# Optimization experiments

Hardware: AMD Instinct MI355X
Metric: run time of the kernel (lower is better)

## Reference

```python
import jax, jax.numpy as jnp
import numpy as np
from jax import lax

DEPTH = 12
NUM_HEADS = 12
WINDOW = 14
GLOBAL_IDX = (2, 5, 8, 11)
EPS = 1e-6


def setup_inputs() -> dict:
    key = jax.random.key(0)
    ks = iter(jax.random.split(key, 64))
    def rn(shape, s=0.02):
        return jax.random.normal(next(ks), shape, jnp.float32) * s
    D, mlp, hd = 768, 3072, 64
    return dict(
        x=jax.random.normal(next(ks), (1, 3, 512, 512), jnp.float32),
        patch_w=rn((D, 3, 16, 16)), patch_b=rn((D,)),
        pos_embed=rn((1, 32, 32, D)),
        ln1_w=jnp.ones((DEPTH, D)), ln1_b=jnp.zeros((DEPTH, D)),
        qkv_w=rn((DEPTH, D, 3 * D)), qkv_b=rn((DEPTH, 3 * D)),
        proj_w=rn((DEPTH, D, D)), proj_b=rn((DEPTH, D)),
        ln2_w=jnp.ones((DEPTH, D)), ln2_b=jnp.zeros((DEPTH, D)),
        mlp1_w=rn((DEPTH, D, mlp)), mlp1_b=rn((DEPTH, mlp)),
        mlp2_w=rn((DEPTH, mlp, D)), mlp2_b=rn((DEPTH, D)),
        rel_h_win=rn((8, 2 * WINDOW - 1, hd)), rel_w_win=rn((8, 2 * WINDOW - 1, hd)),
        rel_h_glob=rn((4, 2 * 32 - 1, hd)), rel_w_glob=rn((4, 2 * 32 - 1, hd)),
        neck_w1=rn((256, D, 1, 1)),
        neck_ln1_w=jnp.ones((256,)), neck_ln1_b=jnp.zeros((256,)),
        neck_w2=rn((256, 256, 3, 3)),
        neck_ln2_w=jnp.ones((256,)), neck_ln2_b=jnp.zeros((256,)),
    )


def layer_norm(x, w, b):
    m = jnp.mean(x, -1, keepdims=True)
    v = jnp.mean(jnp.square(x - m), -1, keepdims=True)
    return (x - m) * lax.rsqrt(v + EPS) * w + b


def layer_norm_2d(x, w, b):
    # channels-first LN over dim 1, as in SAM's LayerNorm2d
    m = jnp.mean(x, 1, keepdims=True)
    v = jnp.mean(jnp.square(x - m), 1, keepdims=True)
    x = (x - m) * lax.rsqrt(v + EPS)
    return x * w[None, :, None, None] + b[None, :, None, None]


def window_partition(x, ws):
    B, H, W, C = x.shape
    ph, pw = (-H) % ws, (-W) % ws
    x = jnp.pad(x, ((0, 0), (0, ph), (0, pw), (0, 0)))
    Hp, Wp = H + ph, W + pw
    x = x.reshape(B, Hp // ws, ws, Wp // ws, ws, C).transpose(0, 1, 3, 2, 4, 5)
    return x.reshape(-1, ws, ws, C), (Hp, Wp)


def window_unpartition(win, ws, pad_hw, hw):
    Hp, Wp = pad_hw
    H, W = hw
    B = win.shape[0] // (Hp * Wp // ws // ws)
    x = win.reshape(B, Hp // ws, Wp // ws, ws, ws, -1).transpose(0, 1, 3, 2, 4, 5)
    x = x.reshape(B, Hp, Wp, -1)
    return x[:, :H, :W, :]


def attention(x, qkv_w, qkv_b, proj_w, proj_b, Rh, Rw):
    B, H, W, C = x.shape
    nh = NUM_HEADS
    hd = C // nh
    scale = hd ** -0.5
    qkv = (x.reshape(B, H * W, C) @ qkv_w + qkv_b).reshape(B, H * W, 3, nh, hd)
    qkv = qkv.transpose(2, 0, 3, 1, 4).reshape(3, B * nh, H * W, hd)
    q, k, v = qkv[0], qkv[1], qkv[2]
    attn = jnp.einsum('bqc,bkc->bqk', q * scale, k)  # (B*nh, HW, HW)
    # decomposed rel-pos (q_size == k_size, no interpolation branch)
    idx_h = jnp.arange(H)[:, None] - jnp.arange(H)[None, :] + (H - 1)
    idx_w = jnp.arange(W)[:, None] - jnp.arange(W)[None, :] + (W - 1)
    Rh_s = Rh[idx_h]  # (H, H, hd)
    Rw_s = Rw[idx_w]  # (W, W, hd)
    r_q = q.reshape(B * nh, H, W, hd)
    rel_h = jnp.einsum('bhwc,hkc->bhwk', r_q, Rh_s)
    rel_w = jnp.einsum('bhwc,wkc->bhwk', r_q, Rw_s)
    attn = attn.reshape(B * nh, H, W, H, W) + rel_h[:, :, :, :, None] + rel_w[:, :, :, None, :]
    attn = jax.nn.softmax(attn.reshape(B * nh, H * W, H * W), axis=-1)
    out = (attn @ v).reshape(B, nh, H, W, hd).transpose(0, 2, 3, 1, 4).reshape(B, H, W, C)
    return out @ proj_w + proj_b


def encoder_forward(x, patch_w, patch_b, pos_embed, ln1_w, ln1_b, qkv_w, qkv_b,
                    proj_w, proj_b, ln2_w, ln2_b, mlp1_w, mlp1_b, mlp2_w, mlp2_b,
                    rel_h_win, rel_w_win, rel_h_glob, rel_w_glob,
                    neck_w1, neck_ln1_w, neck_ln1_b, neck_w2, neck_ln2_w, neck_ln2_b):
    dn = ('NCHW', 'OIHW', 'NCHW')
    # patch embed: conv 16x16 stride 16 -> (B, H', W', C)
    h = lax.conv_general_dilated(x, patch_w, (16, 16), 'VALID', dimension_numbers=dn)
    h = h + patch_b[None, :, None, None]
    h = h.transpose(0, 2, 3, 1)  # (B, 32, 32, 768)
    h = h + pos_embed
    wi = gi = 0
    for i in range(DEPTH):
        shortcut = h
        y = layer_norm(h, ln1_w[i], ln1_b[i])
        if i in GLOBAL_IDX:
            y = attention(y, qkv_w[i], qkv_b[i], proj_w[i], proj_b[i],
                          rel_h_glob[gi], rel_w_glob[gi])
            gi += 1
        else:
            Hh, Ww = y.shape[1], y.shape[2]
            y, pad_hw = window_partition(y, WINDOW)
            y = attention(y, qkv_w[i], qkv_b[i], proj_w[i], proj_b[i],
                          rel_h_win[wi], rel_w_win[wi])
            y = window_unpartition(y, WINDOW, pad_hw, (Hh, Ww))
            wi += 1
        h = shortcut + y
        m = layer_norm(h, ln2_w[i], ln2_b[i])
        m = jax.nn.gelu(m @ mlp1_w[i] + mlp1_b[i], approximate=False) @ mlp2_w[i] + mlp2_b[i]
        h = h + m
    # neck
    h = h.transpose(0, 3, 1, 2)  # (B, C, H, W)
    h = lax.conv_general_dilated(h, neck_w1, (1, 1), 'VALID', dimension_numbers=dn)
    h = layer_norm_2d(h, neck_ln1_w, neck_ln1_b)
    h = lax.conv_general_dilated(h, neck_w2, (1, 1), [(1, 1), (1, 1)], dimension_numbers=dn)
    h = layer_norm_2d(h, neck_ln2_w, neck_ln2_b)
    return h  # (B, 256, 32, 32)


def reference(x, patch_w, patch_b, pos_embed, ln1_w, ln1_b, qkv_w, qkv_b,
              proj_w, proj_b, ln2_w, ln2_b, mlp1_w, mlp1_b, mlp2_w, mlp2_b,
              rel_h_win, rel_w_win, rel_h_glob, rel_w_glob,
              neck_w1, neck_ln1_w, neck_ln1_b, neck_w2, neck_ln2_w, neck_ln2_b):
    return encoder_forward(x, patch_w, patch_b, pos_embed, ln1_w, ln1_b, qkv_w, qkv_b,
                           proj_w, proj_b, ln2_w, ln2_b, mlp1_w, mlp1_b, mlp2_w, mlp2_b,
                           rel_h_win, rel_w_win, rel_h_glob, rel_w_glob,
                           neck_w1, neck_ln1_w, neck_ln1_b, neck_w2, neck_ln2_w, neck_ln2_b)
```

## Files before the change

### kernel.cpp

```cpp
#include <hip/hip_runtime.h>
#include <hip/hip_bf16.h>
#include <math.h>

#define CDIV(a,b) (((a)+(b)-1)/(b))

typedef short bf16x8 __attribute__((ext_vector_type(8)));
typedef float f32x4 __attribute__((ext_vector_type(4)));

__device__ __forceinline__ ushort f2bf(float f){
    __hip_bfloat16 h = __float2bfloat16(f);
    return *reinterpret_cast<ushort*>(&h);
}
__device__ __forceinline__ float bf2f(ushort u){
    __hip_bfloat16 h;
    *reinterpret_cast<ushort*>(&h) = u;
    return __bfloat162float(h);
}

template<int BM, int EPI, bool OUTBF>
__global__ __launch_bounds__(256) void mgemm_k(
    const ushort* __restrict__ A, int lda,
    const ushort* __restrict__ B, int ldb,
    void* __restrict__ Cv, int ldc,
    const float* __restrict__ bias, const float* __restrict__ res,
    int M, int N, int K, float alpha, int nh,
    long sAb, long sAh, long sBb, long sBh, long sCb, long sCh)
{
    constexpr int MI = BM / 32;
    constexpr int ACH = BM / 64;
    constexpr int ABYTES = BM * 64;
    constexpr int DBOF = ABYTES + 4096;

    const int z = blockIdx.z;
    const int bb = z / nh, hh = z - bb * nh;
    A += bb * sAb + hh * sAh;
    B += bb * sBb + hh * sBh;
    const long coff = bb * sCb + hh * sCh;

    __shared__ __align__(16) char smem[2 * DBOF];

    const int tid = threadIdx.x;
    const int m0 = blockIdx.y * BM;
    const int n0 = blockIdx.x * 64;
    const int lane = tid & 63;
    const int w = tid >> 6;
    const int wr = w >> 1, wc = w & 1;
    const int kg = lane >> 4, lr = lane & 15;

    const int rA = tid >> 2, gA = tid & 3;
    const ushort* aptr[ACH]; bool pAv[ACH]; int sAoff[ACH];
    #pragma unroll
    for (int it = 0; it < ACH; ++it) {
        const int gm = m0 + rA + it * 64;
        pAv[it] = gm < M;
        const int cm = pAv[it] ? gm : (M > 0 ? M - 1 : 0);
        aptr[it] = A + (long)cm * lda + (gA << 3);
        sAoff[it] = gA * (BM * 16) + ((rA << 4) ^ (gA << 5)) + it * 1024;
    }
    const int gn_s = n0 + rA;
    const bool pBv = gn_s < N;
    const ushort* bptr = B + (long)(pBv ? gn_s : (N - 1)) * ldb + (gA << 3);
    const int sBoff = ABYTES + gA * 1024 + ((rA << 4) ^ (gA << 5));

    int afoff[MI], bqoff[2];
    #pragma unroll
    for (int mi = 0; mi < MI; ++mi)
        afoff[mi] = kg * (BM * 16) + (((wr * (BM / 2) + mi * 16 + lr) << 4) ^ (kg << 5));
    #pragma unroll
    for (int ni = 0; ni < 2; ++ni)
        bqoff[ni] = ABYTES + kg * 1024 + (((wc * 32 + ni * 16 + lr) << 4) ^ (kg << 5));

    const bf16x8 z8 = {0,0,0,0,0,0,0,0};
    f32x4 acc[MI][2];
    #pragma unroll
    for (int mi = 0; mi < MI; ++mi)
        #pragma unroll
        for (int ni = 0; ni < 2; ++ni)
            acc[mi][ni] = (f32x4){0.f, 0.f, 0.f, 0.f};

    bf16x8 pA[ACH], pB;
    #pragma unroll
    for (int it = 0; it < ACH; ++it)
        pA[it] = pAv[it] ? *(const bf16x8*)(aptr[it]) : z8;
    pB = pBv ? *(const bf16x8*)(bptr) : z8;
    #pragma unroll
    for (int it = 0; it < ACH; ++it) *(bf16x8*)(smem + sAoff[it]) = pA[it];
    *(bf16x8*)(smem + sBoff) = pB;
    __syncthreads();

    const int nt = K >> 5;
    for (int t = 0; t < nt; ++t) {
        const bool more = (t + 1 < nt);
        if (more) {
            const int kn = (t + 1) << 5;
            #pragma unroll
            for (int it = 0; it < ACH; ++it)
                pA[it] = pAv[it] ? *(const bf16x8*)(aptr[it] + kn) : z8;
            pB = pBv ? *(const bf16x8*)(bptr + kn) : z8;
        }
        const char* base = smem + (t & 1) * DBOF;
        bf16x8 af[MI], bq[2];
        #pragma unroll
        for (int mi = 0; mi < MI; ++mi) af[mi] = *(const bf16x8*)(base + afoff[mi]);
        #pragma unroll
        for (int ni = 0; ni < 2; ++ni) bq[ni] = *(const bf16x8*)(base + bqoff[ni]);
        #pragma unroll
        for (int mi = 0; mi < MI; ++mi)
            #pragma unroll
            for (int ni = 0; ni < 2; ++ni)
                acc[mi][ni] = __builtin_amdgcn_mfma_f32_16x16x32_bf16(
                    af[mi], bq[ni], acc[mi][ni], 0, 0, 0);
        if (more) {
            char* dst = smem + ((t + 1) & 1) * DBOF;
            #pragma unroll
            for (int it = 0; it < ACH; ++it) *(bf16x8*)(dst + sAoff[it]) = pA[it];
            *(bf16x8*)(dst + sBoff) = pB;
        }
        __syncthreads();
    }

    #pragma unroll
    for (int mi = 0; mi < MI; ++mi) {
        #pragma unroll
        for (int ni = 0; ni < 2; ++ni) {
            #pragma unroll
            for (int q = 0; q < 4; ++q) {
                const int gm = m0 + wr * (BM / 2) + mi * 16 + kg * 4 + q;
                const int gn = n0 + wc * 32 + ni * 16 + lr;
                if (gm < M && gn < N) {
                    float v = acc[mi][ni][q] * alpha;
                    if (EPI >= 1) v += bias[gn];
                    const long ci = coff + (long)gm * ldc + gn;
                    if (EPI == 2) v = 0.5f * v * (1.0f + erff(v * 0.70710678118654752f));
                    if (EPI == 3) v += res[ci];
                    if (OUTBF) ((ushort*)Cv)[ci] = f2bf(v);
                    else       ((float*)Cv)[ci]  = v;
                }
            }
        }
    }
}

static inline void mgemm(hipStream_t st, int bm, int epi, bool outbf,
                         const ushort* A, int lda, const ushort* B, int ldb,
                         void* C, int ldc, const float* bias, const float* res,
                         int M, int N, int K, float alpha,
                         int batch, int nh,
                         long sAb, long sAh, long sBb, long sBh, long sCb, long sCh)
{
    dim3 g(CDIV(N, 64), CDIV(M, bm), batch);
    dim3 b(256);
#define MG(BMv, E, O) mgemm_k<BMv, E, O><<<g, b, 0, st>>>(A, lda, B, ldb, C, ldc, bias, res, M, N, K, alpha, nh, sAb, sAh, sBb, sBh, sCb, sCh)
    if (bm == 128) {
        if (epi == 0 && !outbf)      MG(128, 0, false);
        else if (epi == 0)           MG(128, 0, true);
        else if (epi == 1 && !outbf) MG(128, 1, false);
        else if (epi == 1)           MG(128, 1, true);
        else if (epi == 2)           MG(128, 2, true);
        else                         MG(128, 3, false);
    } else {
        if (epi == 0 && !outbf)      MG(64, 0, false);
        else if (epi == 0)           MG(64, 0, true);
        else if (epi == 1 && !outbf) MG(64, 1, false);
        else if (epi == 1)           MG(64, 1, true);
        else if (epi == 2)           MG(64, 2, true);
        else                         MG(64, 3, false);
    }
#undef MG
}

__global__ __launch_bounds__(256) void wtrans_k(
    const float* __restrict__ in, ushort* __restrict__ out, int K, int N)
{
    __shared__ float t[32][33];
    const int k0 = blockIdx.y << 5, n0 = blockIdx.x << 5;
    const int tx = threadIdx.x, ty = threadIdx.y;
    #pragma unroll
    for (int j = 0; j < 32; j += 8)
        t[ty + j][tx] = in[(long)(k0 + ty + j) * N + n0 + tx];
    __syncthreads();
    #pragma unroll
    for (int j = 0; j < 32; j += 8)
        out[(long)(n0 + ty + j) * K + k0 + tx] = f2bf(t[tx][ty + j]);
}

__global__ void cvt_k(const float* __restrict__ in, ushort* __restrict__ out, int n)
{
    const int i = blockIdx.x * 256 + threadIdx.x;
    if (i < n) out[i] = f2bf(in[i]);
}

__global__ __launch_bounds__(256) void ln_part_k(
    const float* __restrict__ x, ushort* __restrict__ y,
    const float* __restrict__ w, const float* __restrict__ b, int window)
{
    __shared__ float s1[256], s2[256];
    const int t = blockIdx.x, tid = threadIdx.x;
    int g = t; bool valid = true;
    if (window) {
        const int wi = t / 196, loc = t - wi * 196;
        const int wy = wi / 3, wx = wi - wy * 3;
        const int ly = loc / 14, lx = loc - ly * 14;
        const int gy = wy * 14 + ly, gx = wx * 14 + lx;
        valid = (gy < 32) && (gx < 32);
        g = gy * 32 + gx;
    }
    float xs[3] = {0.f, 0.f, 0.f};
    if (valid) {
        const float* xr = x + (long)g * 768;
        xs[0] = xr[tid]; xs[1] = xr[tid + 256]; xs[2] = xr[tid + 512];
    }
    s1[tid] = xs[0] + xs[1] + xs[2];
    s2[tid] = xs[0] * xs[0] + xs[1] * xs[1] + xs[2] * xs[2];
    __syncthreads();
    for (int off = 128; off > 0; off >>= 1) {
        if (tid < off) { s1[tid] += s1[tid + off]; s2[tid] += s2[tid + off]; }
        __syncthreads();
    }
    const float mean = s1[0] * (1.f / 768.f);
    const float var  = s2[0] * (1.f / 768.f) - mean * mean;
    const float rs   = rsqrtf(var + 1e-6f);
    ushort* yr = y + (long)t * 768;
    if (valid) {
        #pragma unroll
        for (int j = 0; j < 3; ++j) {
            const int c = tid + j * 256;
            yr[c] = f2bf((xs[j] - mean) * rs * w[c] + b[c]);
        }
    } else {
        #pragma unroll
        for (int j = 0; j < 3; ++j) yr[tid + j * 256] = 0;
    }
}

__global__ void scatter_add_k(float* __restrict__ h, const float* __restrict__ src, int window)
{
    const int idx = blockIdx.x * 256 + threadIdx.x;
    if (idx >= 1024 * 768) return;
    const int g = idx / 768, c = idx - g * 768;
    int t = g;
    if (window) {
        const int gy = g >> 5, gx = g & 31;
        const int wy = gy / 14, ly = gy - wy * 14;
        const int wx = gx / 14, lx = gx - wx * 14;
        t = (wy * 3 + wx) * 196 + ly * 14 + lx;
    }
    h[idx] += src[(long)t * 768 + c];
}

__global__ __launch_bounds__(64) void qrel_k(
    const ushort* __restrict__ qkv, const float* __restrict__ Rh, const float* __restrict__ Rw,
    float* __restrict__ relh, float* __restrict__ relw, int S, int H, int nh)
{
    const int row = blockIdx.x;
    const int z = row / S, t = row - z * S;
    const int b = z / nh, hh = z - b * nh;
    const int r = threadIdx.x;
    const int W = H;
    const int qh = t / W, qw = t - qh * W;
    const ushort* q = qkv + ((long)(b * S + t)) * 2304 + hh * 64;
    if (r < H) {
        const float* R = Rh + (long)(qh - r + H - 1) * 64;
        float s = 0.f;
        for (int c = 0; c < 64; ++c) s += bf2f(q[c]) * R[c];
        relh[(long)row * H + r] = s;
    } else if (r < H + W) {
        const int r2 = r - H;
        const float* R = Rw + (long)(qw - r2 + W - 1) * 64;
        float s = 0.f;
        for (int c = 0; c < 64; ++c) s += bf2f(q[c]) * R[c];
        relw[(long)row * W + r2] = s;
    }
}

__global__ __launch_bounds__(256) void softmax_rel_k(
    const float* __restrict__ attn, ushort* __restrict__ probs,
    const float* __restrict__ relh, const float* __restrict__ relw,
    int S, int W, int Spad)
{
    __shared__ float red[256];
    const long row = blockIdx.x;
    const int H = S / W;
    const float* a = attn + row * S;
    const int zz = (int)(row / S), t = (int)(row - (long)zz * S);
    ushort* p = probs + (long)zz * S * Spad + (long)t * Spad;
    const float* rh = relh + row * H;
    const float* rw = relw + row * W;
    const int tid = threadIdx.x;

    float vv[4];
    float mx = -1e30f;
    #pragma unroll
    for (int i = 0; i < 4; ++i) {
        const int j = tid + (i << 8);
        float v = -1e30f;
        if (j < S) {
            const int kh = j / W, kw = j - kh * W;
            v = a[j] + rh[kh] + rw[kw];
        }
        vv[i] = v;
        mx = fmaxf(mx, v);
    }
    red[tid] = mx; __syncthreads();
    for (int off = 128; off > 0; off >>= 1) {
        if (tid < off) red[tid] = fmaxf(red[tid], red[tid + off]);
        __syncthreads();
    }
    mx = red[0]; __syncthreads();
    float sum = 0.f;
    #pragma unroll
    for (int i = 0; i < 4; ++i) {
        const int j = tid + (i << 8);
        if (j < S) { const float e = __expf(vv[i] - mx); vv[i] = e; sum += e; }
    }
    red[tid] = sum; __syncthreads();
    for (int off = 128; off > 0; off >>= 1) {
        if (tid < off) red[tid] += red[tid + off];
        __syncthreads();
    }
    const float inv = 1.0f / red[0];
    #pragma unroll
    for (int i = 0; i < 4; ++i) {
        const int j = tid + (i << 8);
        if (j < S) p[j] = f2bf(vv[i] * inv);
    }
    for (int j = S + tid; j < Spad; j += 256) p[j] = 0;
}

__global__ void vT_k(const ushort* __restrict__ qkv, ushort* __restrict__ vT,
                     int S, int Spad, int total)
{
    const int idx = blockIdx.x * 256 + threadIdx.x;
    if (idx >= total) return;
    const int z = idx / (64 * Spad);
    const int rem = idx - z * 64 * Spad;
    const int c = rem / Spad, t = rem - c * Spad;
    const int bb = z / 12, hh = z - bb * 12;
    ushort v = 0;
    if (t < S) v = qkv[((long)(bb * S + t)) * 2304 + 1536 + hh * 64 + c];
    vT[idx] = v;
}

__global__ void im2col_patch_k(const float* __restrict__ x, ushort* __restrict__ xc)
{
    const int idx = blockIdx.x * 256 + threadIdx.x;
    if (idx >= 1024 * 768) return;
    const int t = idx / 768, k = idx - t * 768;
    const int ph = t >> 5, pw = t & 31;
    const int c = k >> 8, rem = k & 255;
    const int kh = rem >> 4, kw = rem & 15;
    xc[idx] = f2bf(x[((long)c * 512 + (ph * 16 + kh)) * 512 + (pw * 16 + kw)]);
}

__global__ void add_pos_k(float* __restrict__ h, const float* __restrict__ pos)
{
    const int idx = blockIdx.x * 256 + threadIdx.x;
    if (idx < 1024 * 768) h[idx] += pos[idx];
}

__global__ void im2col_neck_k(const float* __restrict__ in, ushort* __restrict__ xc)
{
    const int idx = blockIdx.x * 256 + threadIdx.x;
    if (idx >= 1024 * 2304) return;
    const int p = idx / 2304, k = idx - p * 2304;
    const int ci = k / 9, r = k - ci * 9;
    const int kh = r / 3, kw = r - kh * 3;
    const int gy = (p >> 5) + kh - 1, gx = (p & 31) + kw - 1;
    float v = 0.f;
    if (gy >= 0 && gy < 32 && gx >= 0 && gx < 32)
        v = in[((long)(gy * 32 + gx)) * 256 + ci];
    xc[idx] = f2bf(v);
}

__global__ __launch_bounds__(256) void ln2d_k(
    const float* __restrict__ x, float* __restrict__ y,
    const float* __restrict__ w, const float* __restrict__ b, int chw_out)
{
    __shared__ float s1[256], s2[256];
    const int p = blockIdx.x, c = threadIdx.x;
    const float v = x[(long)p * 256 + c];
    s1[c] = v; s2[c] = v * v;
    __syncthreads();
    for (int off = 128; off > 0; off >>= 1) {
        if (c < off) { s1[c] += s1[c + off]; s2[c] += s2[c + off]; }
        __syncthreads();
    }
    const float mean = s1[0] * (1.f / 256.f);
    const float var  = s2[0] * (1.f / 256.f) - mean * mean;
    const float out  = (v - mean) * rsqrtf(var + 1e-6f) * w[c] + b[c];
    if (chw_out) y[(long)c * 1024 + p] = out;
    else         y[(long)p * 256 + c] = out;
}

extern "C" void kernel_launch(void* const* d_in, const int* in_sizes, int n_in,
                              void* d_out, int out_size, void* d_ws, size_t ws_size,
                              hipStream_t stream)
{
    const float* x       = (const float*)d_in[0];
    const float* patch_w = (const float*)d_in[1];
    const float* patch_b = (const float*)d_in[2];
    const float* pos     = (const float*)d_in[3];
    const float* ln1_w   = (const float*)d_in[4];
    const float* ln1_b   = (const float*)d_in[5];
    const float* qkv_w   = (const float*)d_in[6];
    const float* qkv_b   = (const float*)d_in[7];
    const float* proj_w  = (const float*)d_in[8];
    const float* proj_b  = (const float*)d_in[9];
    const float* ln2_w   = (const float*)d_in[10];
    const float* ln2_b   = (const float*)d_in[11];
    const float* mlp1_w  = (const float*)d_in[12];
    const float* mlp1_b  = (const float*)d_in[13];
    const float* mlp2_w  = (const float*)d_in[14];
    const float* mlp2_b  = (const float*)d_in[15];
    const float* rhw     = (const float*)d_in[16];
    const float* rww     = (const float*)d_in[17];
    const float* rhg     = (const float*)d_in[18];
    const float* rwg     = (const float*)d_in[19];
    const float* neck_w1 = (const float*)d_in[20];
    const float* nln1_w  = (const float*)d_in[21];
    const float* nln1_b  = (const float*)d_in[22];
    const float* neck_w2 = (const float*)d_in[23];
    const float* nln2_w  = (const float*)d_in[24];
    const float* nln2_b  = (const float*)d_in[25];
    (void)in_sizes; (void)n_in; (void)out_size; (void)ws_size;

    char* cur = (char*)d_ws;
    auto alloc = [&](size_t bytes) -> char* {
        char* p = cur; cur += (bytes + 255) & ~(size_t)255; return p;
    };
    float*  h      = (float*) alloc(1024l * 768 * 4);
    ushort* ybf    = (ushort*)alloc(1764l * 768 * 2);
    ushort* qkvbf  = (ushort*)alloc(1764l * 2304 * 2);
    float*  attn   = (float*) alloc(12l * 1024 * 1024 * 4);
    ushort* probs  = (ushort*)alloc(12l * 1024 * 1024 * 2);
    ushort* obf    = (ushort*)alloc(1764l * 768 * 2);
    float*  tb     = (float*) alloc(1024l * 3072 * 4);
    float*  relh   = (float*) alloc(12l * 1024 * 32 * 4);
    float*  relw   = (float*) alloc(12l * 1024 * 32 * 4);
    ushort* vT     = (ushort*)alloc(108l * 64 * 224 * 2);
    ushort* qkvT   = (ushort*)alloc(2304l * 768 * 2);
    ushort* projT  = (ushort*)alloc(768l * 768 * 2);
    ushort* m1T    = (ushort*)alloc(3072l * 768 * 2);
    ushort* m2T    = (ushort*)alloc(768l * 3072 * 2);
    ushort* patchbf= (ushort*)alloc(768l * 768 * 2);
    ushort* xc     = (ushort*)alloc(1024l * 768 * 2);
    ushort* xcn    = (ushort*)alloc(1024l * 2304 * 2);
    ushort* hbf    = (ushort*)alloc(1024l * 768 * 2);
    ushort* nw1bf  = (ushort*)alloc(256l * 768 * 2);
    ushort* nw2bf  = (ushort*)alloc(256l * 2304 * 2);
    float*  nk1    = (float*) alloc(1024l * 256 * 4);
    float*  nk2    = (float*) alloc(1024l * 256 * 4);

    cvt_k<<<CDIV(768 * 768, 256), 256, 0, stream>>>(patch_w, patchbf, 768 * 768);
    cvt_k<<<CDIV(256 * 768, 256), 256, 0, stream>>>(neck_w1, nw1bf, 256 * 768);
    cvt_k<<<CDIV(256 * 2304, 256), 256, 0, stream>>>(neck_w2, nw2bf, 256 * 2304);

    im2col_patch_k<<<CDIV(786432, 256), 256, 0, stream>>>(x, xc);
    mgemm(stream, 64, 1, false, xc, 768, patchbf, 768, h, 768, patch_b, nullptr,
          1024, 768, 768, 1.f, 1, 1, 0, 0, 0, 0, 0, 0);
    add_pos_k<<<CDIV(786432, 256), 256, 0, stream>>>(h, pos);

    int wi = 0, gi = 0;
    for (int i = 0; i < 12; ++i) {
        const bool glb = (i == 2) || (i == 5) || (i == 8) || (i == 11);
        const int S  = glb ? 1024 : 196;
        const int Spad = glb ? 1024 : 224;
        const int nB = glb ? 1 : 9;
        const int ntok = nB * S;
        const int HH = glb ? 32 : 14;
        const int Z  = nB * 12;

        wtrans_k<<<dim3(2304/32, 768/32),  dim3(32,8), 0, stream>>>(qkv_w  + (long)i*768*2304, qkvT, 768, 2304);
        wtrans_k<<<dim3(768/32,  768/32),  dim3(32,8), 0, stream>>>(proj_w + (long)i*768*768,  projT, 768, 768);
        wtrans_k<<<dim3(3072/32, 768/32),  dim3(32,8), 0, stream>>>(mlp1_w + (long)i*768*3072, m1T,  768, 3072);
        wtrans_k<<<dim3(768/32,  3072/32), dim3(32,8), 0, stream>>>(mlp2_w + (long)i*3072*768, m2T, 3072, 768);

        ln_part_k<<<ntok, 256, 0, stream>>>(h, ybf, ln1_w + i*768, ln1_b + i*768, glb ? 0 : 1);
        mgemm(stream, 128, 1, true, ybf, 768, qkvT, 768, qkvbf, 2304, qkv_b + i*2304, nullptr,
              ntok, 2304, 768, 1.f, 1, 1, 0, 0, 0, 0, 0, 0);
        mgemm(stream, glb ? 128 : 64, 0, false, qkvbf, 2304, qkvbf + 768, 2304, attn, S, nullptr, nullptr,
              S, S, 64, 0.125f, Z, 12,
              (long)S * 2304, 64, (long)S * 2304, 64, (long)12 * S * S, (long)S * S);
        const float* Rh = glb ? (rhg + (long)gi * 63 * 64) : (rhw + (long)wi * 27 * 64);
        const float* Rw = glb ? (rwg + (long)gi * 63 * 64) : (rww + (long)wi * 27 * 64);
        qrel_k<<<Z * S, 64, 0, stream>>>(qkvbf, Rh, Rw, relh, relw, S, HH, 12);
        {
            const int tot = Z * 64 * Spad;
            vT_k<<<CDIV(tot, 256), 256, 0, stream>>>(qkvbf, vT, S, Spad, tot);
        }
        softmax_rel_k<<<Z * S, 256, 0, stream>>>(attn, probs, relh, relw, S, HH, Spad);
        mgemm(stream, 64, 0, true, probs, Spad, vT, Spad, obf, 768, nullptr, nullptr,
              S, 64, Spad, 1.f, Z, 12,
              (long)12 * S * Spad, (long)S * Spad, (long)12 * 64 * Spad, (long)64 * Spad,
              (long)S * 768, 64);
        mgemm(stream, 64, 1, false, obf, 768, projT, 768, tb, 768, proj_b + i*768, nullptr,
              ntok, 768, 768, 1.f, 1, 1, 0, 0, 0, 0, 0, 0);
        scatter_add_k<<<CDIV(786432, 256), 256, 0, stream>>>(h, tb, glb ? 0 : 1);
        ln_part_k<<<1024, 256, 0, stream>>>(h, ybf, ln2_w + i*768, ln2_b + i*768, 0);
        mgemm(stream, 128, 2, true, ybf, 768, m1T, 768, tb, 3072, mlp1_b + i*3072, nullptr,
              1024, 3072, 768, 1.f, 1, 1, 0, 0, 0, 0, 0, 0);
        mgemm(stream, 64, 3, false, (ushort*)tb, 3072, m2T, 3072, h, 768, mlp2_b + i*768, h,
              1024, 768, 3072, 1.f, 1, 1, 0, 0, 0, 0, 0, 0);

        if (glb) gi++; else wi++;
    }

    cvt_k<<<CDIV(786432, 256), 256, 0, stream>>>(h, hbf, 786432);
    mgemm(stream, 64, 0, false, hbf, 768, nw1bf, 768, nk1, 256, nullptr, nullptr,
          1024, 256, 768, 1.f, 1, 1, 0, 0, 0, 0, 0, 0);
    ln2d_k<<<1024, 256, 0, stream>>>(nk1, nk2, nln1_w, nln1_b, 0);
    im2col_neck_k<<<CDIV(1024 * 2304, 256), 256, 0, stream>>>(nk2, xcn);
    mgemm(stream, 64, 0, false, xcn, 2304, nw2bf, 2304, nk1, 256, nullptr, nullptr,
          1024, 256, 2304, 1.f, 1, 1, 0, 0, 0, 0, 0, 0);
    ln2d_k<<<1024, 256, 0, stream>>>(nk1, (float*)d_out, nln2_w, nln2_b, 1);
}
```

Measured before the change: 2.954 ms.

## Fuse attention into flash-style kernel, fuse residual with LN, batch weight transposes

Replaces the separate QK^T GEMM, relative-position softmax, and PV GEMM with a single flash-attention kernel. It uses MFMA and online softmax with swizzled LDS tiles, so the full fp32 score and bf16 probability matrices are never written to memory. It also fuses the post-attention residual scatter-add with the second LayerNorm, and transposes all layer weights in four batched launches up front instead of per layer. The fused attention uses small 128-thread blocks and reloads K/V per 32-query tile, which may limit occupancy and reuse.

```diff
diff --git a/kernel.cpp b/kernel.cpp
--- a/kernel.cpp
+++ b/kernel.cpp
@@ -169,10 +169,162 @@
 #undef MG
 }
 
-__global__ __launch_bounds__(256) void wtrans_k(
+__global__ __launch_bounds__(128) void fattn_k(
+    const ushort* __restrict__ qkv, const ushort* __restrict__ vT,
+    const float* __restrict__ relh, const float* __restrict__ relw,
+    ushort* __restrict__ obf, int S, int Spad, int HH, int nh)
+{
+    const int z = blockIdx.y;
+    const int bb = z / nh, hh = z - bb * nh;
+    const int qt0 = blockIdx.x * 32;
+    const int tid = threadIdx.x;
+    const int lane = tid & 63;
+    const int w = tid >> 6;
+    const int lr = lane & 15, kg = lane >> 4;
+    const bf16x8 z8 = {0,0,0,0,0,0,0,0};
+
+    __shared__ __align__(16) char smem[20480];
+    char* sK  = smem;
+    char* sVT = smem + 8192;
+    char* sP  = smem + 16384 + w * 2048;
+
+    const int qrow = qt0 + w * 16 + lr;
+    const bool qv = qrow < S;
+    const ushort* qp = qkv + ((long)(bb * S + (qv ? qrow : 0))) * 2304 + hh * 64 + (kg << 3);
+    bf16x8 qf[2];
+    qf[0] = qv ? *(const bf16x8*)(qp)      : z8;
+    qf[1] = qv ? *(const bf16x8*)(qp + 32) : z8;
+
+    f32x4 m = {-1e30f, -1e30f, -1e30f, -1e30f};
+    f32x4 l = {0.f, 0.f, 0.f, 0.f};
+    f32x4 o[4];
+    #pragma unroll
+    for (int i = 0; i < 4; ++i) o[i] = (f32x4){0.f, 0.f, 0.f, 0.f};
+
+    const int trow0 = qt0 + w * 16 + kg * 4;
+    const long relbase = ((long)z * S + trow0) * HH;
+
+    for (int c0 = 0; c0 < S; c0 += 64) {
+        __syncthreads();
+        #pragma unroll
+        for (int it = 0; it < 4; ++it) {
+            const int cc = tid + it * 128;
+            const int n = cc >> 3, ch = cc & 7;
+            const int kb = ch >> 2, g = ch & 3;
+            const int tok = c0 + n;
+            bf16x8 v = z8;
+            if (tok < S)
+                v = *(const bf16x8*)(qkv + ((long)(bb * S + tok)) * 2304 + 768 + hh * 64 + ch * 8);
+            *(bf16x8*)(sK + kb * 4096 + g * 1024 + ((n << 4) ^ (g << 5))) = v;
+        }
+        #pragma unroll
+        for (int it = 0; it < 4; ++it) {
+            const int cc = tid + it * 128;
+            const int d = cc >> 3, ch = cc & 7;
+            const int kb = ch >> 2, g = ch & 3;
+            const int key = c0 + ch * 8;
+            bf16x8 v = z8;
+            if (key < Spad)
+                v = *(const bf16x8*)(vT + ((long)(z * 64 + d)) * Spad + key);
+            *(bf16x8*)(sVT + kb * 4096 + g * 1024 + ((d << 4) ^ (g << 5))) = v;
+        }
+        __syncthreads();
+
+        f32x4 s[4];
+        #pragma unroll
+        for (int ntl = 0; ntl < 4; ++ntl) s[ntl] = (f32x4){0.f, 0.f, 0.f, 0.f};
+        #pragma unroll
+        for (int stp = 0; stp < 2; ++stp) {
+            #pragma unroll
+            for (int ntl = 0; ntl < 4; ++ntl) {
+                const bf16x8 kf = *(const bf16x8*)(sK + stp * 4096 + kg * 1024 +
+                                   (((ntl * 16 + lr) << 4) ^ (kg << 5)));
+                s[ntl] = __builtin_amdgcn_mfma_f32_16x16x32_bf16(qf[stp], kf, s[ntl], 0, 0, 0);
+            }
+        }
+        #pragma unroll
+        for (int ntl = 0; ntl < 4; ++ntl) {
+            const int j = c0 + ntl * 16 + lr;
+            #pragma unroll
+            for (int qi = 0; qi < 4; ++qi) {
+                const int t = trow0 + qi;
+                float v;
+                if (t < S && j < S) {
+                    const int kh = j / HH, kw = j - kh * HH;
+                    const long rb = relbase + (long)qi * HH;
+                    v = s[ntl][qi] * 0.125f + relh[rb + kh] + relw[rb + kw];
+                } else v = -1e30f;
+                s[ntl][qi] = v;
+            }
+        }
+        f32x4 mn, rsum, sc;
+        #pragma unroll
+        for (int qi = 0; qi < 4; ++qi) {
+            float r = fmaxf(fmaxf(s[0][qi], s[1][qi]), fmaxf(s[2][qi], s[3][qi]));
+            #pragma unroll
+            for (int d = 1; d < 16; d <<= 1) r = fmaxf(r, __shfl_xor(r, d, 16));
+            mn[qi] = fmaxf(m[qi], r);
+        }
+        #pragma unroll
+        for (int qi = 0; qi < 4; ++qi) {
+            float sum = 0.f;
+            #pragma unroll
+            for (int ntl = 0; ntl < 4; ++ntl) {
+                const float e = __expf(s[ntl][qi] - mn[qi]);
+                s[ntl][qi] = e;
+                sum += e;
+            }
+            #pragma unroll
+            for (int d = 1; d < 16; d <<= 1) sum += __shfl_xor(sum, d, 16);
+            rsum[qi] = sum;
+            sc[qi] = __expf(m[qi] - mn[qi]);
+            l[qi] = l[qi] * sc[qi] + rsum[qi];
+            m[qi] = mn[qi];
+        }
+        #pragma unroll
+        for (int ntl = 0; ntl < 4; ++ntl) o[ntl] = o[ntl] * sc;
+
+        #pragma unroll
+        for (int ntl = 0; ntl < 4; ++ntl) {
+            #pragma unroll
+            for (int qi = 0; qi < 4; ++qi) {
+                const int r = kg * 4 + qi;
+                *(ushort*)(sP + r * 128 + ((((ntl * 16 + lr) << 1)) ^ ((r >> 2) << 5))) =
+                    f2bf(s[ntl][qi]);
+            }
+        }
+        #pragma unroll
+        for (int stp = 0; stp < 2; ++stp) {
+            const bf16x8 pa = *(const bf16x8*)(sP + lr * 128 +
+                               (((stp * 64 + kg * 16)) ^ ((lr >> 2) << 5)));
+            #pragma unroll
+            for (int ntd = 0; ntd < 4; ++ntd) {
+                const bf16x8 vb = *(const bf16x8*)(sVT + stp * 4096 + kg * 1024 +
+                                   (((ntd * 16 + lr) << 4) ^ (kg << 5)));
+                o[ntd] = __builtin_amdgcn_mfma_f32_16x16x32_bf16(pa, vb, o[ntd], 0, 0, 0);
+            }
+        }
+    }
+
+    #pragma unroll
+    for (int qi = 0; qi < 4; ++qi) {
+        const int t = trow0 + qi;
+        if (t < S) {
+            const float inv = 1.0f / l[qi];
+            ushort* op = obf + ((long)(bb * S + t)) * 768 + hh * 64 + lr;
+            #pragma unroll
+            for (int ntd = 0; ntd < 4; ++ntd)
+                op[ntd * 16] = f2bf(o[ntd][qi] * inv);
+        }
+    }
+}
+
+__global__ __launch_bounds__(256) void wtrans_all_k(
     const float* __restrict__ in, ushort* __restrict__ out, int K, int N)
 {
     __shared__ float t[32][33];
+    const long loff = (long)blockIdx.z * K * N;
+    in += loff; out += loff;
     const int k0 = blockIdx.y << 5, n0 = blockIdx.x << 5;
     const int tx = threadIdx.x, ty = threadIdx.y;
     #pragma unroll
@@ -233,11 +385,12 @@
     }
 }
 
-__global__ void scatter_add_k(float* __restrict__ h, const float* __restrict__ src, int window)
-{
-    const int idx = blockIdx.x * 256 + threadIdx.x;
-    if (idx >= 1024 * 768) return;
-    const int g = idx / 768, c = idx - g * 768;
+__global__ __launch_bounds__(256) void res_ln_k(
+    float* __restrict__ h, const float* __restrict__ src, int window,
+    const float* __restrict__ w, const float* __restrict__ b, ushort* __restrict__ y)
+{
+    __shared__ float s1[256], s2[256];
+    const int g = blockIdx.x, tid = threadIdx.x;
     int t = g;
     if (window) {
         const int gy = g >> 5, gx = g & 31;
@@ -245,7 +398,28 @@
         const int wx = gx / 14, lx = gx - wx * 14;
         t = (wy * 3 + wx) * 196 + ly * 14 + lx;
     }
-    h[idx] += src[(long)t * 768 + c];
+    float xs[3];
+    #pragma unroll
+    for (int j = 0; j < 3; ++j) {
+        const int c = tid + j * 256;
+        xs[j] = h[(long)g * 768 + c] + src[(long)t * 768 + c];
+        h[(long)g * 768 + c] = xs[j];
+    }
+    s1[tid] = xs[0] + xs[1] + xs[2];
+    s2[tid] = xs[0] * xs[0] + xs[1] * xs[1] + xs[2] * xs[2];
+    __syncthreads();
+    for (int off = 128; off > 0; off >>= 1) {
+        if (tid < off) { s1[tid] += s1[tid + off]; s2[tid] += s2[tid + off]; }
+        __syncthreads();
+    }
+    const float mean = s1[0] * (1.f / 768.f);
+    const float var  = s2[0] * (1.f / 768.f) - mean * mean;
+    const float rs   = rsqrtf(var + 1e-6f);
+    #pragma unroll
+    for (int j = 0; j < 3; ++j) {
+        const int c = tid + j * 256;
+        y[(long)g * 768 + c] = f2bf((xs[j] - mean) * rs * w[c] + b[c]);
+    }
 }
 
 __global__ __launch_bounds__(64) void qrel_k(
@@ -271,60 +445,6 @@
         for (int c = 0; c < 64; ++c) s += bf2f(q[c]) * R[c];
         relw[(long)row * W + r2] = s;
     }
-}
-
-__global__ __launch_bounds__(256) void softmax_rel_k(
-    const float* __restrict__ attn, ushort* __restrict__ probs,
-    const float* __restrict__ relh, const float* __restrict__ relw,
-    int S, int W, int Spad)
-{
-    __shared__ float red[256];
-    const long row = blockIdx.x;
-    const int H = S / W;
-    const float* a = attn + row * S;
-    const int zz = (int)(row / S), t = (int)(row - (long)zz * S);
-    ushort* p = probs + (long)zz * S * Spad + (long)t * Spad;
-    const float* rh = relh + row * H;
-    const float* rw = relw + row * W;
-    const int tid = threadIdx.x;
-
-    float vv[4];
-    float mx = -1e30f;
-    #pragma unroll
-    for (int i = 0; i < 4; ++i) {
-        const int j = tid + (i << 8);
-        float v = -1e30f;
-        if (j < S) {
-            const int kh = j / W, kw = j - kh * W;
-            v = a[j] + rh[kh] + rw[kw];
-        }
-        vv[i] = v;
-        mx = fmaxf(mx, v);
-    }
-    red[tid] = mx; __syncthreads();
-    for (int off = 128; off > 0; off >>= 1) {
-        if (tid < off) red[tid] = fmaxf(red[tid], red[tid + off]);
-        __syncthreads();
-    }
-    mx = red[0]; __syncthreads();
-    float sum = 0.f;
-    #pragma unroll
-    for (int i = 0; i < 4; ++i) {
-        const int j = tid + (i << 8);
-        if (j < S) { const float e = __expf(vv[i] - mx); vv[i] = e; sum += e; }
-    }
-    red[tid] = sum; __syncthreads();
-    for (int off = 128; off > 0; off >>= 1) {
-        if (tid < off) red[tid] += red[tid + off];
-        __syncthreads();
-    }
-    const float inv = 1.0f / red[0];
-    #pragma unroll
-    for (int i = 0; i < 4; ++i) {
-        const int j = tid + (i << 8);
-        if (j < S) p[j] = f2bf(vv[i] * inv);
-    }
-    for (int j = S + tid; j < Spad; j += 256) p[j] = 0;
 }
 
 __global__ void vT_k(const ushort* __restrict__ qkv, ushort* __restrict__ vT,
@@ -431,17 +551,15 @@
     float*  h      = (float*) alloc(1024l * 768 * 4);
     ushort* ybf    = (ushort*)alloc(1764l * 768 * 2);
     ushort* qkvbf  = (ushort*)alloc(1764l * 2304 * 2);
-    float*  attn   = (float*) alloc(12l * 1024 * 1024 * 4);
-    ushort* probs  = (ushort*)alloc(12l * 1024 * 1024 * 2);
     ushort* obf    = (ushort*)alloc(1764l * 768 * 2);
     float*  tb     = (float*) alloc(1024l * 3072 * 4);
     float*  relh   = (float*) alloc(12l * 1024 * 32 * 4);
     float*  relw   = (float*) alloc(12l * 1024 * 32 * 4);
     ushort* vT     = (ushort*)alloc(108l * 64 * 224 * 2);
-    ushort* qkvT   = (ushort*)alloc(2304l * 768 * 2);
-    ushort* projT  = (ushort*)alloc(768l * 768 * 2);
-    ushort* m1T    = (ushort*)alloc(3072l * 768 * 2);
-    ushort* m2T    = (ushort*)alloc(768l * 3072 * 2);
+    ushort* qkvT   = (ushort*)alloc(12l * 2304 * 768 * 2);
+    ushort* projT  = (ushort*)alloc(12l * 768 * 768 * 2);
+    ushort* m1T    = (ushort*)alloc(12l * 3072 * 768 * 2);
+    ushort* m2T    = (ushort*)alloc(12l * 768 * 3072 * 2);
     ushort* patchbf= (ushort*)alloc(768l * 768 * 2);
     ushort* xc     = (ushort*)alloc(1024l * 768 * 2);
     ushort* xcn    = (ushort*)alloc(1024l * 2304 * 2);
@@ -454,6 +572,10 @@
     cvt_k<<<CDIV(768 * 768, 256), 256, 0, stream>>>(patch_w, patchbf, 768 * 768);
     cvt_k<<<CDIV(256 * 768, 256), 256, 0, stream>>>(neck_w1, nw1bf, 256 * 768);
     cvt_k<<<CDIV(256 * 2304, 256), 256, 0, stream>>>(neck_w2, nw2bf, 256 * 2304);
+    wtrans_all_k<<<dim3(2304/32, 768/32, 12),  dim3(32,8), 0, stream>>>(qkv_w,  qkvT, 768, 2304);
+    wtrans_all_k<<<dim3(768/32,  768/32, 12),  dim3(32,8), 0, stream>>>(proj_w, projT, 768, 768);
+    wtrans_all_k<<<dim3(3072/32, 768/32, 12),  dim3(32,8), 0, stream>>>(mlp1_w, m1T,  768, 3072);
+    wtrans_all_k<<<dim3(768/32,  3072/32, 12), dim3(32,8), 0, stream>>>(mlp2_w, m2T, 3072, 768);
 
     im2col_patch_k<<<CDIV(786432, 256), 256, 0, stream>>>(x, xc);
     mgemm(stream, 64, 1, false, xc, 768, patchbf, 768, h, 768, patch_b, nullptr,
@@ -470,17 +592,9 @@
         const int HH = glb ? 32 : 14;
         const int Z  = nB * 12;
 
-        wtrans_k<<<dim3(2304/32, 768/32),  dim3(32,8), 0, stream>>>(qkv_w  + (long)i*768*2304, qkvT, 768, 2304);
-        wtrans_k<<<dim3(768/32,  768/32),  dim3(32,8), 0, stream>>>(proj_w + (long)i*768*768,  projT, 768, 768);
-        wtrans_k<<<dim3(3072/32, 768/32),  dim3(32,8), 0, stream>>>(mlp1_w + (long)i*768*3072, m1T,  768, 3072);
-        wtrans_k<<<dim3(768/32,  3072/32), dim3(32,8), 0, stream>>>(mlp2_w + (long)i*3072*768, m2T, 3072, 768);
-
         ln_part_k<<<ntok, 256, 0, stream>>>(h, ybf, ln1_w + i*768, ln1_b + i*768, glb ? 0 : 1);
-        mgemm(stream, 128, 1, true, ybf, 768, qkvT, 768, qkvbf, 2304, qkv_b + i*2304, nullptr,
-              ntok, 2304, 768, 1.f, 1, 1, 0, 0, 0, 0, 0, 0);
-        mgemm(stream, glb ? 128 : 64, 0, false, qkvbf, 2304, qkvbf + 768, 2304, attn, S, nullptr, nullptr,
-              S, S, 64, 0.125f, Z, 12,
-              (long)S * 2304, 64, (long)S * 2304, 64, (long)12 * S * S, (long)S * S);
+        mgemm(stream, 128, 1, true, ybf, 768, qkvT + (long)i*2304*768, 768, qkvbf, 2304,
+              qkv_b + i*2304, nullptr, ntok, 2304, 768, 1.f, 1, 1, 0, 0, 0, 0, 0, 0);
         const float* Rh = glb ? (rhg + (long)gi * 63 * 64) : (rhw + (long)wi * 27 * 64);
         const float* Rw = glb ? (rwg + (long)gi * 63 * 64) : (rww + (long)wi * 27 * 64);
         qrel_k<<<Z * S, 64, 0, stream>>>(qkvbf, Rh, Rw, relh, relw, S, HH, 12);
@@ -488,19 +602,16 @@
             const int tot = Z * 64 * Spad;
             vT_k<<<CDIV(tot, 256), 256, 0, stream>>>(qkvbf, vT, S, Spad, tot);
         }
-        softmax_rel_k<<<Z * S, 256, 0, stream>>>(attn, probs, relh, relw, S, HH, Spad);
-        mgemm(stream, 64, 0, true, probs, Spad, vT, Spad, obf, 768, nullptr, nullptr,
-              S, 64, Spad, 1.f, Z, 12,
-              (long)12 * S * Spad, (long)S * Spad, (long)12 * 64 * Spad, (long)64 * Spad,
-              (long)S * 768, 64);
-        mgemm(stream, 64, 1, false, obf, 768, projT, 768, tb, 768, proj_b + i*768, nullptr,
-              ntok, 768, 768, 1.f, 1, 1, 0, 0, 0, 0, 0, 0);
-        scatter_add_k<<<CDIV(786432, 256), 256, 0, stream>>>(h, tb, glb ? 0 : 1);
-        ln_part_k<<<1024, 256, 0, stream>>>(h, ybf, ln2_w + i*768, ln2_b + i*768, 0);
-        mgemm(stream, 128, 2, true, ybf, 768, m1T, 768, tb, 3072, mlp1_b + i*3072, nullptr,
-              1024, 3072, 768, 1.f, 1, 1, 0, 0, 0, 0, 0, 0);
-        mgemm(stream, 64, 3, false, (ushort*)tb, 3072, m2T, 3072, h, 768, mlp2_b + i*768, h,
-              1024, 768, 3072, 1.f, 1, 1, 0, 0, 0, 0, 0, 0);
+        fattn_k<<<dim3(CDIV(S, 32), Z), 128, 0, stream>>>(
+            qkvbf, vT, relh, relw, obf, S, Spad, HH, 12);
+        mgemm(stream, 64, 1, false, obf, 768, projT + (long)i*768*768, 768, tb, 768,
+              proj_b + i*768, nullptr, ntok, 768, 768, 1.f, 1, 1, 0, 0, 0, 0, 0, 0);
+        res_ln_k<<<1024, 256, 0, stream>>>(h, tb, glb ? 0 : 1,
+                                           ln2_w + i*768, ln2_b + i*768, ybf);
+        mgemm(stream, 128, 2, true, ybf, 768, m1T + (long)i*3072*768, 768, tb, 3072,
+              mlp1_b + i*3072, nullptr, 1024, 3072, 768, 1.f, 1, 1, 0, 0, 0, 0, 0, 0);
+        mgemm(stream, 64, 3, false, (ushort*)tb, 3072, m2T + (long)i*768*3072, 3072, h, 768,
+              mlp2_b + i*768, h, 1024, 768, 3072, 1.f, 1, 1, 0, 0, 0, 0, 0, 0);
 
         if (glb) gi++; else wi++;
     }
```

Measured after the change: 2.852 ms. 1.04x faster.
